# Kernel tuning notes

Hardware: AMD Instinct MI355X
Metric: run time of the kernel (lower is better)

The kernel has to match this reference:

```python
import jax, jax.numpy as jnp
import numpy as np

OBS_LEN, PRED_LEN, N, P = 8, 12, 4096, 32
EH, DH, EMB, BOT, NZ = 64, 128, 64, 1024, 8


def setup_inputs() -> dict:
    key = jax.random.key(0)
    ks = iter(jax.random.split(key, 64))
    rn = lambda shp, s=0.05: (jax.random.normal(next(ks), shp, jnp.float32) * s)
    d = {
        'obs_traj': rn((OBS_LEN, N, 2), 1.0),
        'obs_traj_rel': rn((OBS_LEN, N, 2), 0.5),
        'obs_speed': jax.random.uniform(next(ks), (OBS_LEN, N, 1), jnp.float32),
        'noise': rn((N, NZ), 1.0),
        'enc_emb_W': rn((2, EMB)), 'enc_emb_b': jnp.zeros((EMB,), jnp.float32),
        'enc_Wih': rn((EMB, 4 * EH)), 'enc_Whh': rn((EH, 4 * EH)), 'enc_b': jnp.zeros((4 * EH,), jnp.float32),
        'pool_sp_W': rn((2, 64)), 'pool_sp_b': jnp.zeros((64,), jnp.float32),
        'pool_spd_W': rn((1, 64)), 'pool_spd_b': jnp.zeros((64,), jnp.float32),
        'pool_l1_W': rn((192, 512)), 'pool_l1_b': jnp.zeros((512,), jnp.float32),
        'pool_bn1_g': jnp.ones((512,), jnp.float32), 'pool_bn1_b': jnp.zeros((512,), jnp.float32),
        'pool_l2_W': rn((512, BOT)), 'pool_l2_b': jnp.zeros((BOT,), jnp.float32),
        'pool_bn2_g': jnp.ones((BOT,), jnp.float32), 'pool_bn2_b': jnp.zeros((BOT,), jnp.float32),
        'spd_emb_W': rn((OBS_LEN, 64)), 'spd_emb_b': jnp.zeros((64,), jnp.float32),
        'ctx_l1_W': rn((EH + BOT + 64, 1024)), 'ctx_l1_b': jnp.zeros((1024,), jnp.float32),
        'ctx_bn1_g': jnp.ones((1024,), jnp.float32), 'ctx_bn1_b': jnp.zeros((1024,), jnp.float32),
        'ctx_l2_W': rn((1024, DH - NZ)), 'ctx_l2_b': jnp.zeros((DH - NZ,), jnp.float32),
        'ctx_bn2_g': jnp.ones((DH - NZ,), jnp.float32), 'ctx_bn2_b': jnp.zeros((DH - NZ,), jnp.float32),
        'dec_emb_W': rn((3, EMB)), 'dec_emb_b': jnp.zeros((EMB,), jnp.float32),
        'dec_Wih': rn((EMB, 4 * DH)), 'dec_Whh': rn((DH, 4 * DH)), 'dec_b': jnp.zeros((4 * DH,), jnp.float32),
        'h2p_W': rn((DH, 2)), 'h2p_b': jnp.zeros((2,), jnp.float32),
        'group_size': P,
    }
    return d


def _lstm(xs, Wih, Whh, b, h0, c0):
    # xs: [T, B, in]; PyTorch gate order (i, f, g, o)
    def step(carry, x):
        h, c = carry
        g = x @ Wih + h @ Whh + b
        i, f, gg, o = jnp.split(g, 4, axis=-1)
        c = jax.nn.sigmoid(f) * c + jax.nn.sigmoid(i) * jnp.tanh(gg)
        h = jax.nn.sigmoid(o) * jnp.tanh(c)
        return (h, c), h
    (h, c), _ = jax.lax.scan(step, (h0, c0), xs)
    return h, c


def _bn(x, g, b):
    # BatchNorm1d, eval mode with running_mean=0, running_var=1
    return x * g + b


def reference(obs_traj, obs_traj_rel, obs_speed, noise,
              enc_emb_W, enc_emb_b, enc_Wih, enc_Whh, enc_b,
              pool_sp_W, pool_sp_b, pool_spd_W, pool_spd_b,
              pool_l1_W, pool_l1_b, pool_bn1_g, pool_bn1_b,
              pool_l2_W, pool_l2_b, pool_bn2_g, pool_bn2_b,
              spd_emb_W, spd_emb_b,
              ctx_l1_W, ctx_l1_b, ctx_bn1_g, ctx_bn1_b,
              ctx_l2_W, ctx_l2_b, ctx_bn2_g, ctx_bn2_b,
              dec_emb_W, dec_emb_b, dec_Wih, dec_Whh, dec_b,
              h2p_W, h2p_b, group_size):
    n = obs_traj.shape[1]
    G = n // group_size
    # ---- Encoder: embed rel traj, run LSTM, take final hidden ----
    emb = obs_traj_rel @ enc_emb_W + enc_emb_b                       # [T, N, 64]
    h0 = jnp.zeros((n, EH), emb.dtype)
    final_h, _ = _lstm(emb, enc_Wih, enc_Whh, enc_b, h0, h0)         # [N, 64]
    # ---- PoolHiddenNet (vectorized per-group P x P social pooling) ----
    end_pos = obs_traj[-1].reshape(G, group_size, 2)                 # [G, P, 2]
    end_spd = obs_speed[-1].reshape(G, group_size, 1)                # [G, P, 1]
    hG = final_h.reshape(G, group_size, EH)                          # [G, P, 64]
    # rel[g, i, j] = pos[g, j] - pos[g, i]
    rel = end_pos[:, None, :, :] - end_pos[:, :, None, :]            # [G, P, P, 2]
    rel_e = rel @ pool_sp_W + pool_sp_b                              # [G, P, P, 64]
    spd_e = end_spd @ pool_spd_W + pool_spd_b                        # [G, P, 64]
    Pn = group_size
    feat = jnp.concatenate([
        rel_e,
        jnp.broadcast_to(hG[:, None, :, :], (G, Pn, Pn, EH)),
        jnp.broadcast_to(spd_e[:, None, :, :], (G, Pn, Pn, 64)),
    ], axis=-1)                                                      # [G, P, P, 192]
    h1 = jax.nn.relu(_bn(feat @ pool_l1_W + pool_l1_b, pool_bn1_g, pool_bn1_b))
    h2 = jax.nn.relu(_bn(h1 @ pool_l2_W + pool_l2_b, pool_bn2_g, pool_bn2_b))
    pool_h = jnp.max(h2, axis=2).reshape(n, BOT)                     # max over j -> [N, 1024]
    # ---- speed context: sigmoid(Linear(8 -> 64)) over obs speed history ----
    spd_hist = jnp.transpose(obs_speed[:, :, 0])                     # [N, 8]
    speed_ctx = jax.nn.sigmoid(spd_hist @ spd_emb_W + spd_emb_b)     # [N, 64]
    # ---- mlp_decoder_context + ped-level noise ----
    ctx_in = jnp.concatenate([final_h, pool_h, speed_ctx], axis=1)   # [N, 1152]
    c1 = jax.nn.relu(_bn(ctx_in @ ctx_l1_W + ctx_l1_b, ctx_bn1_g, ctx_bn1_b))
    ctx = jax.nn.relu(_bn(c1 @ ctx_l2_W + ctx_l2_b, ctx_bn2_g, ctx_bn2_b))  # [N, 120]
    dec_h = jnp.concatenate([ctx, noise], axis=1)                    # [N, 128]
    dec_c = jnp.zeros_like(dec_h)
    # ---- Decoder rollout (pred_len steps) ----
    last_pos = obs_traj[-1]
    last_speed = obs_speed[-1]                                       # [N, 1]
    x0 = jnp.concatenate([obs_traj_rel[-1], last_speed], axis=1) @ dec_emb_W + dec_emb_b

    def step(carry, _):
        h, c, x, lp = carry
        g = x @ dec_Wih + h @ dec_Whh + dec_b
        i, f, gg, o = jnp.split(g, 4, axis=-1)
        c = jax.nn.sigmoid(f) * c + jax.nn.sigmoid(i) * jnp.tanh(gg)
        h = jax.nn.sigmoid(o) * jnp.tanh(c)
        rel_pos = h @ h2p_W + h2p_b                                  # [N, 2]
        cur = rel_pos + lp
        x = jnp.concatenate([rel_pos, last_speed], axis=1) @ dec_emb_W + dec_emb_b
        return (h, c, x, cur), rel_pos

    _, rels = jax.lax.scan(step, (dec_h, dec_c, x0, last_pos), None, length=PRED_LEN)
    return rels  # [pred_len, N, 2]
```

## Files before the change

kernel.cpp:

```cpp
#include <hip/hip_runtime.h>

typedef __attribute__((ext_vector_type(8))) short v8s;
typedef __attribute__((ext_vector_type(4))) float v4f;
typedef unsigned short u16;

#define DINL static __device__ __forceinline__

DINL float b2f(u16 u){ union { unsigned uu; float ff; } x; x.uu = ((unsigned)u)<<16; return x.ff; }
DINL u16 f2b(float f){ union { float ff; unsigned uu; } x; x.ff = f; unsigned r = x.uu + 0x7FFFu + ((x.uu>>16)&1u); return (u16)(r>>16); }
DINL float sigm(float x){ return 1.0f/(1.0f+__expf(-x)); }
DINL float tanh_(float x){ return 2.0f/(1.0f+__expf(-2.0f*x)) - 1.0f; }
DINL float ld(const void* p, int i, int isf){
    return isf ? ((const float*)p)[i] : b2f(((const u16*)p)[i]);
}
DINL void g2lds16(const u16* g, u16* l){
    __builtin_amdgcn_global_load_lds(
        (const __attribute__((address_space(1))) unsigned int*)g,
        (__attribute__((address_space(3))) unsigned int*)l, 16, 0, 0);
}

#define FLAG_OFF 0x000000
#define AUX_OFF  0x000100
#define ENCF_OFF 0x010000
#define DECF_OFF 0x020000
#define CW2T_OFF 0x050000
#define W2T_OFF  0x090000
#define DECH_OFF 0x090000
#define CW1T_OFF 0x190000
#define IT_OFF   0x3D0000
#define IR_OFF   0x3F0000
#define IS_OFF   0x410000
#define INZ_OFF  0x420000
#define IW1H_OFF 0x430000
#define SM_OFF   0x440000
#define CTX_OFF  0x450000
#define AV_OFF   0xD50000
#define BIG_NEED 0x1550000

#define SM_EEW 0
#define SM_EEB 128
#define SM_ENB 192
#define SM_DEW 448
#define SM_DEB 640
#define SM_DNB 704
#define SM_H2W 1216
#define SM_H2B 1472
#define SM_SEW 1536
#define SM_SEB 2048

__global__ void k_detect(const void* obs_speed, int* flag){
    if (threadIdx.x == 0 && blockIdx.x == 0){
        const u16* p = (const u16*)obs_speed;
        int f = 0;
        for (int i = 0; i < 16; ++i){
            u16 v = p[2*i];
            if ((v & 0x8000u) || v > 0x3F80u) f = 1;
        }
        *flag = f;
    }
}

__global__ __launch_bounds__(256) void k_conv_inp(
    const void* obs_traj, const void* obs_rel, const void* obs_speed, const void* noise,
    const void* pool_l1_W,
    const void* eeW, const void* eeB, const void* encB,
    const void* deW, const void* deB, const void* decB,
    const void* h2W, const void* h2B, const void* seW, const void* seB,
    const int* flag, u16* IT, u16* IR, u16* IS, u16* INZ, u16* IW1H, u16* SM)
{
    const int isf = *flag;
    int idx = blockIdx.x*256 + threadIdx.x;
    if (idx < 65536){ IT[idx] = f2b(ld(obs_traj, idx, isf)); return; }
    idx -= 65536;
    if (idx < 65536){ IR[idx] = f2b(ld(obs_rel, idx, isf)); return; }
    idx -= 65536;
    if (idx < 32768){ IS[idx] = f2b(ld(obs_speed, idx, isf)); return; }
    idx -= 32768;
    if (idx < 32768){ INZ[idx] = f2b(ld(noise, idx, isf)); return; }
    idx -= 32768;
    if (idx < 32768){ IW1H[idx] = f2b(ld(pool_l1_W, idx + 32768, isf)); return; }
    idx -= 32768;
    if (idx < 128){ SM[SM_EEW + idx] = f2b(ld(eeW, idx, isf)); return; }
    idx -= 128;
    if (idx < 64){ SM[SM_EEB + idx] = f2b(ld(eeB, idx, isf)); return; }
    idx -= 64;
    if (idx < 256){ SM[SM_ENB + idx] = f2b(ld(encB, idx, isf)); return; }
    idx -= 256;
    if (idx < 192){ SM[SM_DEW + idx] = f2b(ld(deW, idx, isf)); return; }
    idx -= 192;
    if (idx < 64){ SM[SM_DEB + idx] = f2b(ld(deB, idx, isf)); return; }
    idx -= 64;
    if (idx < 512){ SM[SM_DNB + idx] = f2b(ld(decB, idx, isf)); return; }
    idx -= 512;
    if (idx < 256){ SM[SM_H2W + idx] = f2b(ld(h2W, idx, isf)); return; }
    idx -= 256;
    if (idx < 2){ SM[SM_H2B + idx] = f2b(ld(h2B, idx, isf)); return; }
    idx -= 2;
    if (idx < 512){ SM[SM_SEW + idx] = f2b(ld(seW, idx, isf)); return; }
    idx -= 512;
    if (idx < 64){ SM[SM_SEB + idx] = f2b(ld(seB, idx, isf)); return; }
}

__global__ __launch_bounds__(256) void k_trans(
    const void* __restrict__ in, u16* __restrict__ out,
    int K, int N, const int* __restrict__ flag)
{
    __shared__ float tile[64][65];
    const int isf = *flag;
    const int nbase = blockIdx.x*64, kbase = blockIdx.y*64;
    const int c = threadIdx.x & 63, r0 = (threadIdx.x >> 6)*16;
    for (int rep = 0; rep < 16; ++rep){
        int r = r0 + rep;
        int n = nbase + c;
        float v = 0.f;
        if (n < N) v = ld(in, (kbase + r)*N + n, isf);
        tile[r][c] = v;
    }
    __syncthreads();
    for (int rep = 0; rep < 16; ++rep){
        int r = r0 + rep;
        out[(size_t)(nbase + r)*K + kbase + c] = f2b(tile[c][r]);
    }
}

__global__ __launch_bounds__(256) void k_prep_frag(
    const void* __restrict__ enc_Wih, const void* __restrict__ enc_Whh,
    const void* __restrict__ dec_Wih, const void* __restrict__ dec_Whh,
    const int* flag, u16* __restrict__ encF, u16* __restrict__ decF)
{
    const int isf = *flag;
    int idx = blockIdx.x*256 + threadIdx.x;
    if (idx < 32768){
        int jj = idx&7, lane = (idx>>3)&63, kcnf = idx>>9;
        int kc = kcnf&3, nf = kcnf>>2;
        int k = kc*32 + (lane>>4)*8 + jj, n = nf*16 + (lane&15);
        encF[idx] = (k < 64) ? f2b(ld(enc_Wih, k*256+n, isf)) : f2b(ld(enc_Whh, (k-64)*256+n, isf));
        return;
    }
    idx -= 32768;
    {
        int jj = idx&7, lane = (idx>>3)&63, kcnf = idx>>9;
        int kc = kcnf % 6, nf = kcnf / 6;
        int k = kc*32 + (lane>>4)*8 + jj, n = nf*16 + (lane&15);
        decF[idx] = (k < 64) ? f2b(ld(dec_Wih, k*512+n, isf)) : f2b(ld(dec_Whh, (k-64)*512+n, isf));
    }
}

__global__ __launch_bounds__(256) void k_prep_small(
    const void* __restrict__ spW, const void* __restrict__ spB,
    const void* __restrict__ spdW, const void* __restrict__ spdB,
    const void* __restrict__ l1W, const void* __restrict__ l1B,
    const void* __restrict__ bn1g, const void* __restrict__ bn1b,
    const void* __restrict__ l2b, const void* __restrict__ bn2g, const void* __restrict__ bn2b,
    const void* __restrict__ c1b, const void* __restrict__ cbn1g, const void* __restrict__ cbn1b,
    const void* __restrict__ c2b, const void* __restrict__ cbn2g, const void* __restrict__ cbn2b,
    const int* flag, float* __restrict__ AUX)
{
    const int isf = *flag;
    int idx = blockIdx.x*256 + threadIdx.x;
    if (idx < 512){
        int c = idx;
        float m0 = 0.f, m1 = 0.f, qv = 0.f, cv = 0.f;
        for (int e = 0; e < 64; ++e){
            float w1a = ld(l1W, e*512 + c, isf);
            m0 += ld(spW, e, isf)*w1a;
            m1 += ld(spW, 64+e, isf)*w1a;
            cv += ld(spB, e, isf)*w1a;
            float w1c = ld(l1W, (128+e)*512 + c, isf);
            qv += ld(spdW, e, isf)*w1c;
            cv += ld(spdB, e, isf)*w1c;
        }
        cv += ld(l1B, c, isf);
        float g1 = ld(bn1g, c, isf), bb1 = ld(bn1b, c, isf);
        AUX[c] = m0; AUX[512+c] = m1; AUX[1024+c] = qv; AUX[1536+c] = cv;
        AUX[2048+c] = g1; AUX[2560+c] = bb1;
        AUX[3072+c] = g1*m0; AUX[3584+c] = g1*m1;
        return;
    }
    idx -= 512;
    if (idx < 1024){
        float g = ld(bn2g, idx, isf);
        AUX[4096+idx] = g; AUX[5120+idx] = ld(l2b, idx, isf)*g + ld(bn2b, idx, isf);
        return;
    }
    idx -= 1024;
    if (idx < 1024){
        float g = ld(cbn1g, idx, isf);
        AUX[6144+idx] = g; AUX[7168+idx] = ld(c1b, idx, isf)*g + ld(cbn1b, idx, isf);
        return;
    }
    idx -= 1024;
    if (idx < 128){
        int c = idx;
        float g  = (c < 120) ? ld(cbn2g, c, isf) : 1.f;
        float bb = (c < 120) ? (ld(c2b, c, isf)*g + ld(cbn2b, c, isf)) : 0.f;
        AUX[8192+c] = g; AUX[8320+c] = bb;
    }
}

__global__ __launch_bounds__(256) void k_encoder(
    const u16* __restrict__ rel, const u16* __restrict__ embW, const u16* __restrict__ embB,
    const u16* __restrict__ encF, const u16* __restrict__ encB,
    u16* __restrict__ ctxIn)
{
    __shared__ __align__(16) u16 Als[16*136];
    const int t = threadIdx.x, pedbase = blockIdx.x*16;
    const int w = t>>6, lane = t&63, quad = lane>>4, l15 = lane&15;
    for (int idx = t; idx < 16*64; idx += 256){ int p = idx>>6, jj = idx&63; Als[p*136 + 64 + jj] = 0; }
    {
        int p = t>>4, e0 = (t&15)*4;
        float rx = b2f(rel[(pedbase+p)*2 + 0]);
        float ry = b2f(rel[(pedbase+p)*2 + 1]);
        for (int e = e0; e < e0+4; ++e)
            Als[p*136 + e] = f2b(rx*b2f(embW[e]) + ry*b2f(embW[64+e]) + b2f(embB[e]));
    }
    const int j = w*16 + l15;
    const float bi = b2f(encB[j]), bff = b2f(encB[64+j]), bg = b2f(encB[128+j]), bo = b2f(encB[192+j]);
    float c4[4] = {0.f,0.f,0.f,0.f};
    for (int step = 0; step < 8; ++step){
        __syncthreads();
        v4f acc[4];
        for (int q = 0; q < 4; ++q) acc[q] = (v4f){0.f,0.f,0.f,0.f};
        for (int kc = 0; kc < 4; ++kc){
            v8s a = *(const v8s*)&Als[l15*136 + kc*32 + quad*8];
            for (int q = 0; q < 4; ++q){
                int nf = q*4 + w;
                v8s b = *(const v8s*)&encF[((nf*4 + kc)*64 + lane)*8];
                acc[q] = __builtin_amdgcn_mfma_f32_16x16x32_bf16(a, b, acc[q], 0, 0, 0);
            }
        }
        __syncthreads();
        for (int r = 0; r < 4; ++r){
            float gi = sigm(acc[0][r] + bi), gf = sigm(acc[1][r] + bff);
            float gg = tanh_(acc[2][r] + bg), go = sigm(acc[3][r] + bo);
            c4[r] = gf*c4[r] + gi*gg;
            Als[(quad*4 + r)*136 + 64 + j] = f2b(go*tanh_(c4[r]));
        }
        if (step < 7){
            int p = t>>4, e0 = (t&15)*4;
            float rx = b2f(rel[(step+1)*8192 + (pedbase+p)*2 + 0]);
            float ry = b2f(rel[(step+1)*8192 + (pedbase+p)*2 + 1]);
            for (int e = e0; e < e0+4; ++e)
                Als[p*136 + e] = f2b(rx*b2f(embW[e]) + ry*b2f(embW[64+e]) + b2f(embB[e]));
        }
    }
    __syncthreads();
    for (int idx = t; idx < 1024; idx += 256){
        int p = idx>>6, e = idx&63;
        ctxIn[(size_t)(pedbase+p)*1152 + e] = Als[p*136 + 64 + e];
    }
}

__global__ __launch_bounds__(256) void k_avec(
    const u16* __restrict__ ctxIn, const u16* __restrict__ obs_traj,
    const u16* __restrict__ obs_speed, const u16* __restrict__ IW1H,
    const u16* __restrict__ sW, const u16* __restrict__ sB,
    const float* __restrict__ AUX, u16* __restrict__ Avec, u16* __restrict__ ctxOut)
{
    __shared__ float hs[8][64];
    __shared__ float pxs[8], pys[8], sps[8];
    const int t = threadIdx.x, pedbase = blockIdx.x*8;
    for (int idx = t; idx < 512; idx += 256){
        int p = idx>>6, e = idx&63;
        hs[p][e] = b2f(ctxIn[(size_t)(pedbase+p)*1152 + e]);
    }
    if (t < 8){
        pxs[t] = b2f(obs_traj[7*8192 + (pedbase+t)*2 + 0]);
        pys[t] = b2f(obs_traj[7*8192 + (pedbase+t)*2 + 1]);
        sps[t] = b2f(obs_speed[7*4096 + pedbase + t]);
    }
    __syncthreads();
    const int c0 = (t&127)*4, pg = (t>>7)*4;
    float4 acc[4];
    for (int p = 0; p < 4; ++p) acc[p] = make_float4(0.f,0.f,0.f,0.f);
    for (int e = 0; e < 64; ++e){
        ushort4 wv = *(const ushort4*)(IW1H + e*512 + c0);
        float w0 = b2f(wv.x), w1 = b2f(wv.y), w2 = b2f(wv.z), w3 = b2f(wv.w);
        for (int p = 0; p < 4; ++p){
            float h = hs[pg+p][e];
            acc[p].x += h*w0; acc[p].y += h*w1; acc[p].z += h*w2; acc[p].w += h*w3;
        }
    }
    float4 m0 = *(const float4*)(AUX + c0),        m1 = *(const float4*)(AUX + 512 + c0);
    float4 qv = *(const float4*)(AUX + 1024 + c0), cv = *(const float4*)(AUX + 1536 + c0);
    float4 g1 = *(const float4*)(AUX + 2048 + c0), bb = *(const float4*)(AUX + 2560 + c0);
    for (int p = 0; p < 4; ++p){
        float px = pxs[pg+p], py = pys[pg+p], sp = sps[pg+p];
        ushort4 o;
        o.x = f2b(g1.x*(px*m0.x + py*m1.x + sp*qv.x + cv.x + acc[p].x) + bb.x);
        o.y = f2b(g1.y*(px*m0.y + py*m1.y + sp*qv.y + cv.y + acc[p].y) + bb.y);
        o.z = f2b(g1.z*(px*m0.z + py*m1.z + sp*qv.z + cv.z + acc[p].z) + bb.z);
        o.w = f2b(g1.w*(px*m0.w + py*m1.w + sp*qv.w + cv.w + acc[p].w) + bb.w);
        *(ushort4*)&Avec[(size_t)(pedbase+pg+p)*512 + c0] = o;
    }
    {
        int s = t & 63;
        for (int rep = 0; rep < 2; ++rep){
            int p = (t>>6)*2 + rep;
            int nid = pedbase + p;
            float a = b2f(sB[s]);
            for (int tt = 0; tt < 8; ++tt) a += b2f(obs_speed[tt*4096 + nid]) * b2f(sW[tt*64 + s]);
            ctxOut[(size_t)nid*1152 + 1088 + s] = f2b(sigm(a));
        }
    }
}

__global__ __launch_bounds__(256, 2) void k_pool(
    const u16* __restrict__ Avec, const u16* __restrict__ W2T,
    const u16* __restrict__ IT, const float* __restrict__ AUX,
    u16* __restrict__ ctxIn)
{
    __shared__ __align__(16) u16 Als[64*72];
    __shared__ __align__(16) u16 Bls[512*64];
    __shared__ float auxM[1024];
    __shared__ float pxs[2], pys[2];
    const int t = threadIdx.x;
    const int g = blockIdx.x >> 4, ip = blockIdx.x & 15;
    const int n0 = blockIdx.y * 512;
    const int w = t>>6, lane = t&63, quad = lane>>4, l15 = lane&15;
    const int rw = w>>1, cw = w&1;
    const int aj = t>>3, ao = t&7;
    for (int i = t; i < 1024; i += 256) auxM[i] = AUX[3072 + i];
    if (t < 2){
        pxs[t] = b2f(IT[7*8192 + (g*32 + ip*2 + t)*2 + 0]);
        pys[t] = b2f(IT[7*8192 + (g*32 + ip*2 + t)*2 + 1]);
    }
    const int lgr = (lane&7) ^ (lane>>3);
    const u16* bsrc = W2T + (size_t)(n0 + w*8 + (lane>>3))*512 + lgr*8;
    u16* bdst = &Bls[w*512];
    const u16* arow = Avec + (size_t)(g*32+aj)*512 + ao*8;
    v4f acc[2][16];
    for (int mf = 0; mf < 2; ++mf) for (int nf = 0; nf < 16; ++nf) acc[mf][nf] = (v4f){0.f,0.f,0.f,0.f};
    for (int ch = 0; ch < 8; ++ch){
        const int k0 = ch*64;
        __syncthreads();
        for (int it = 0; it < 16; ++it)
            g2lds16(bsrc + k0 + it*16384, bdst + it*2048);
        {
            union { v8s v; u16 u[8]; } av;
            av.v = *(const v8s*)(arow + k0);
            float a[8], m0a[8], m1a[8];
            for (int i = 0; i < 8; ++i){
                a[i] = b2f(av.u[i]);
                m0a[i] = auxM[k0 + ao*8 + i];
                m1a[i] = auxM[512 + k0 + ao*8 + i];
            }
            for (int il = 0; il < 2; ++il){
                float npx = -pxs[il], npy = -pys[il];
                union { v8s v; u16 u[8]; } pk;
                for (int i = 0; i < 8; ++i){
                    float v = __builtin_fmaf(npy, m1a[i], __builtin_fmaf(npx, m0a[i], a[i]));
                    pk.u[i] = f2b(fmaxf(v, 0.f));
                }
                *(v8s*)&Als[(il*32+aj)*72 + ao*8] = pk.v;
            }
        }
        __syncthreads();
        for (int kc = 0; kc < 2; ++kc){
            v8s af[2];
            for (int mf = 0; mf < 2; ++mf)
                af[mf] = *(const v8s*)&Als[(rw*32 + mf*16 + l15)*72 + kc*32 + quad*8];
            const int pq = ((kc*4 + quad) ^ (l15&7))*8;
            const u16* bbase = &Bls[(cw*256 + l15)*64 + pq];
            #pragma unroll
            for (int nf = 0; nf < 16; ++nf){
                v8s bf = *(const v8s*)(bbase + nf*1024);
                acc[0][nf] = __builtin_amdgcn_mfma_f32_16x16x32_bf16(af[0], bf, acc[0][nf], 0, 0, 0);
                acc[1][nf] = __builtin_amdgcn_mfma_f32_16x16x32_bf16(af[1], bf, acc[1][nf], 0, 0, 0);
            }
        }
    }
    const float* S2 = AUX + 4096; const float* B2 = AUX + 5120;
    for (int nf = 0; nf < 16; ++nf){
        int n = n0 + cw*256 + nf*16 + l15;
        float s = S2[n], bb = B2[n];
        float mm = 0.f;
        for (int mf = 0; mf < 2; ++mf)
            for (int r = 0; r < 4; ++r)
                mm = fmaxf(mm, fmaxf(s*acc[mf][nf][r] + bb, 0.f));
        mm = fmaxf(mm, __shfl_xor(mm, 16));
        mm = fmaxf(mm, __shfl_xor(mm, 32));
        if (quad == 0) ctxIn[(size_t)(g*32 + ip*2 + rw)*1152 + 64 + n] = f2b(mm);
    }
}

template<int MF>
__global__ __launch_bounds__(256) void k_gemm_bt(
    const u16* __restrict__ A, int lda, const u16* __restrict__ BT,
    const float* __restrict__ S, const float* __restrict__ Bb,
    u16* __restrict__ out, int ldo, int K, int validN,
    const u16* __restrict__ noisep)
{
    __shared__ __align__(16) u16 Als[MF*32*72];
    __shared__ __align__(16) u16 Bls[128*72];
    const int t = threadIdx.x;
    const int m0 = blockIdx.x*(MF*32), n0 = blockIdx.y*128;
    const int w = t>>6, lane = t&63, quad = lane>>4, l15 = lane&15;
    const int rw = w>>1, cw = w&1;
    v4f acc[MF][4];
    for (int mf = 0; mf < MF; ++mf) for (int nf = 0; nf < 4; ++nf) acc[mf][nf] = (v4f){0.f,0.f,0.f,0.f};
    const int nch = K >> 6;
    for (int ch = 0; ch < nch; ++ch){
        const int k0 = ch*64;
        __syncthreads();
        if (MF == 4){
// ... 87 lines not shown
        v4f acc[4][2];
        for (int q = 0; q < 4; ++q) for (int nfl = 0; nfl < 2; ++nfl) acc[q][nfl] = (v4f){0.f,0.f,0.f,0.f};
        for (int kc = 0; kc < 6; ++kc){
            v8s a = *(const v8s*)&Als[l15*200 + kc*32 + quad*8];
            for (int q = 0; q < 4; ++q){
                for (int nfl = 0; nfl < 2; ++nfl){
                    int nf = q*8 + w*2 + nfl;
                    v8s b = *(const v8s*)&decF[((nf*6 + kc)*64 + lane)*8];
                    acc[q][nfl] = __builtin_amdgcn_mfma_f32_16x16x32_bf16(a, b, acc[q][nfl], 0, 0, 0);
                }
            }
        }
        __syncthreads();
        for (int nfl = 0; nfl < 2; ++nfl){
            int j = w*32 + nfl*16 + l15;
            for (int r = 0; r < 4; ++r){
                float gi = sigm(acc[0][nfl][r] + bI[nfl]), gf = sigm(acc[1][nfl][r] + bF[nfl]);
                float gg = tanh_(acc[2][nfl][r] + bG[nfl]), go = sigm(acc[3][nfl][r] + bO[nfl]);
                c8[nfl][r] = gf*c8[nfl][r] + gi*gg;
                Als[(quad*4 + r)*200 + 64 + j] = f2b(go*tanh_(c8[nfl][r]));
            }
        }
        __syncthreads();
        if (t < 32){
            int p = t>>1, cmp = t&1;
            float rp = b2f(h2pB[cmp]);
            for (int jj = 0; jj < 128; ++jj) rp += b2f(Als[p*200 + 64 + jj]) * h2ps[jj*2 + cmp];
            int oi = s*8192 + (pedbase+p)*2 + cmp;
            if (isf) ((float*)outp)[oi] = rp;
            else     ((u16*)outp)[oi]   = f2b(rp);
            rps[p][cmp] = rp;
        }
        __syncthreads();
        {
            int p = t>>4, e0 = (t&15)*4;
            for (int e = e0; e < e0+4; ++e){
                float v = rps[p][0]*b2f(dembW[e]) + rps[p][1]*b2f(dembW[64+e]) + sps[p]*b2f(dembW[128+e]) + b2f(dembB[e]);
                Als[p*200 + e] = f2b(v);
            }
        }
    }
}

extern "C" void kernel_launch(void* const* d_in, const int* in_sizes, int n_in,
                              void* d_out, int out_size, void* d_ws, size_t ws_size,
                              hipStream_t stream)
{
    (void)in_sizes; (void)n_in; (void)out_size;
    const void* obs_traj  = d_in[0];
    const void* obs_rel   = d_in[1];
    const void* obs_speed = d_in[2];
    const void* noise     = d_in[3];
    const void* enc_emb_W = d_in[4];
    const void* enc_emb_b = d_in[5];
// ... 30 lines not shown
    const void* h2p_W     = d_in[36];
    const void* h2p_b     = d_in[37];

    char* ws = (char*)d_ws;
    int*   flag  = (int*)  (ws + FLAG_OFF);
    float* AUX   = (float*)(ws + AUX_OFF);
    u16*   encF  = (u16*)  (ws + ENCF_OFF);
    u16*   decF  = (u16*)  (ws + DECF_OFF);
    u16*   cW2T  = (u16*)  (ws + CW2T_OFF);
    u16*   W2T   = (u16*)  (ws + W2T_OFF);
    u16*   decH  = (u16*)  (ws + DECH_OFF);
    u16*   cW1T  = (u16*)  (ws + CW1T_OFF);
    u16*   IT    = (u16*)  (ws + IT_OFF);
    u16*   IR    = (u16*)  (ws + IR_OFF);
    u16*   IS    = (u16*)  (ws + IS_OFF);
    u16*   INZ   = (u16*)  (ws + INZ_OFF);
    u16*   IW1H  = (u16*)  (ws + IW1H_OFF);
    u16*   SM    = (u16*)  (ws + SM_OFF);
    u16*   ctxIn = (u16*)  (ws + CTX_OFF);
    u16*   Avec  = (u16*)  (ws + AV_OFF);
    u16*   c1    = (u16*)  (ws + AV_OFF);
    const bool big = (ws_size >= (size_t)BIG_NEED);

    k_detect<<<dim3(1), dim3(64), 0, stream>>>(obs_speed, flag);
    k_conv_inp<<<dim3(905), dim3(256), 0, stream>>>(
        obs_traj, obs_rel, obs_speed, noise, pool_l1_W,
        enc_emb_W, enc_emb_b, enc_b, dec_emb_W, dec_emb_b, dec_b,
        h2p_W, h2p_b, spd_emb_W, spd_emb_b,
        flag, IT, IR, IS, INZ, IW1H, SM);
    k_prep_frag<<<dim3(512), dim3(256), 0, stream>>>(
        enc_Wih, enc_Whh, dec_Wih, dec_Whh, flag, encF, decF);
    k_trans<<<dim3(16, 8),  dim3(256), 0, stream>>>(pool_l2_W, W2T, 512, 1024, flag);
    k_trans<<<dim3(16, 18), dim3(256), 0, stream>>>(ctx_l1_W, cW1T, 1152, 1024, flag);
    k_trans<<<dim3(2, 16),  dim3(256), 0, stream>>>(ctx_l2_W, cW2T, 1024, 120, flag);
    k_prep_small<<<dim3(11), dim3(256), 0, stream>>>(
        pool_sp_W, pool_sp_b, pool_spd_W, pool_spd_b,
        pool_l1_W, pool_l1_b, pool_bn1_g, pool_bn1_b,
        pool_l2_b, pool_bn2_g, pool_bn2_b,
        ctx_l1_b, ctx_bn1_g, ctx_bn1_b,
        ctx_l2_b, ctx_bn2_g, ctx_bn2_b, flag, AUX);
    k_encoder<<<dim3(256), dim3(256), 0, stream>>>(
        IR, SM + SM_EEW, SM + SM_EEB, encF, SM + SM_ENB, ctxIn);
    k_avec<<<dim3(512), dim3(256), 0, stream>>>(
        ctxIn, IT, IS, IW1H, SM + SM_SEW, SM + SM_SEB, AUX, Avec, ctxIn);
    k_pool<<<dim3(2048, 2), dim3(256), 0, stream>>>(Avec, W2T, IT, AUX, ctxIn);
    if (big){
        k_gemm_bt<4><<<dim3(32, 8), dim3(256), 0, stream>>>(
            ctxIn, 1152, cW1T, AUX + 6144, AUX + 7168, c1, 1024, 1152, 1024, (const u16*)nullptr);
        k_gemm_bt<2><<<dim3(64, 1), dim3(256), 0, stream>>>(
            c1, 1024, cW2T, AUX + 8192, AUX + 8320, decH, 128, 1024, 120, INZ);
    } else {
        k_gemm_bt<4><<<dim3(16, 8), dim3(256), 0, stream>>>(
            ctxIn, 1152, cW1T, AUX + 6144, AUX + 7168, c1, 1024, 1152, 1024, (const u16*)nullptr);
        k_gemm_bt<2><<<dim3(32, 1), dim3(256), 0, stream>>>(
            c1, 1024, cW2T, AUX + 8192, AUX + 8320, decH, 128, 1024, 120, INZ);
        k_gemm_bt<4><<<dim3(16, 8), dim3(256), 0, stream>>>(
            ctxIn + (size_t)2048*1152, 1152, cW1T, AUX + 6144, AUX + 7168, c1, 1024, 1152, 1024, (const u16*)nullptr);
        k_gemm_bt<2><<<dim3(32, 1), dim3(256), 0, stream>>>(
            c1, 1024, cW2T, AUX + 8192, AUX + 8320, decH + (size_t)2048*128, 128, 1024, 120, INZ + (size_t)2048*8);
    }
    k_decoder<<<dim3(256), dim3(256), 0, stream>>>(
        decH, decF, SM + SM_DNB, SM + SM_DEW, SM + SM_DEB,
        SM + SM_H2W, SM + SM_H2B, IR, IS, flag, d_out);
}
```

Before: 507.7 us.

## Merge prep kernels into one launch, fuse avec into encoder, retile pool

Replaces the detect, convert, fragment-prep, three transpose and small-prep launches with a single k_prep kernel where each block detects the dtype flag itself. Folds the avec computation into the encoder so the hidden state stays in LDS instead of a round trip through global memory. Retiles k_pool to 256 output columns per block with a 4x4 MFMA tile per wave, prefetches the next A chunk, and uses a cheaper round-half-up bf16 conversion. Also parallelises the decoder's h2p dot product across 256 threads with shuffle reductions. The aim is fewer launches and better occupancy; the pool retile doubles the grid and repeats the A-side prologue work per block.

```diff
diff --git a/kernel.cpp b/kernel.cpp
--- a/kernel.cpp
+++ b/kernel.cpp
@@ -8,6 +8,7 @@
 
 DINL float b2f(u16 u){ union { unsigned uu; float ff; } x; x.uu = ((unsigned)u)<<16; return x.ff; }
 DINL u16 f2b(float f){ union { float ff; unsigned uu; } x; x.ff = f; unsigned r = x.uu + 0x7FFFu + ((x.uu>>16)&1u); return (u16)(r>>16); }
+DINL u16 f2b_hu(float f){ union { float ff; unsigned uu; } x; x.ff = f; return (u16)((x.uu + 0x8000u)>>16); }
 DINL float sigm(float x){ return 1.0f/(1.0f+__expf(-x)); }
 DINL float tanh_(float x){ return 2.0f/(1.0f+__expf(-2.0f*x)) - 1.0f; }
 DINL float ld(const void* p, int i, int isf){
@@ -17,6 +18,15 @@
     __builtin_amdgcn_global_load_lds(
         (const __attribute__((address_space(1))) unsigned int*)g,
         (__attribute__((address_space(3))) unsigned int*)l, 16, 0, 0);
+}
+DINL int detect_isf(const void* obs_speed){
+    const u16* p = (const u16*)obs_speed;
+    int f = 0;
+    for (int i = 0; i < 16; ++i){
+        u16 v = p[2*i];
+        if ((v & 0x8000u) || v > 0x3F80u) f = 1;
+    }
+    return f;
 }
 
 #define FLAG_OFF 0x000000
@@ -48,67 +58,11 @@
 #define SM_SEW 1536
 #define SM_SEB 2048
 
-__global__ void k_detect(const void* obs_speed, int* flag){
-    if (threadIdx.x == 0 && blockIdx.x == 0){
-        const u16* p = (const u16*)obs_speed;
-        int f = 0;
-        for (int i = 0; i < 16; ++i){
-            u16 v = p[2*i];
-            if ((v & 0x8000u) || v > 0x3F80u) f = 1;
-        }
-        *flag = f;
-    }
-}
-
-__global__ __launch_bounds__(256) void k_conv_inp(
-    const void* obs_traj, const void* obs_rel, const void* obs_speed, const void* noise,
-    const void* pool_l1_W,
-    const void* eeW, const void* eeB, const void* encB,
-    const void* deW, const void* deB, const void* decB,
-    const void* h2W, const void* h2B, const void* seW, const void* seB,
-    const int* flag, u16* IT, u16* IR, u16* IS, u16* INZ, u16* IW1H, u16* SM)
+DINL void trans_tile(const void* in, u16* out, int K, int N, int isf,
+                     int bx, int by, int t, float tile[64][65])
 {
-    const int isf = *flag;
-    int idx = blockIdx.x*256 + threadIdx.x;
-    if (idx < 65536){ IT[idx] = f2b(ld(obs_traj, idx, isf)); return; }
-    idx -= 65536;
-    if (idx < 65536){ IR[idx] = f2b(ld(obs_rel, idx, isf)); return; }
-    idx -= 65536;
-    if (idx < 32768){ IS[idx] = f2b(ld(obs_speed, idx, isf)); return; }
-    idx -= 32768;
-    if (idx < 32768){ INZ[idx] = f2b(ld(noise, idx, isf)); return; }
-    idx -= 32768;
-    if (idx < 32768){ IW1H[idx] = f2b(ld(pool_l1_W, idx + 32768, isf)); return; }
-    idx -= 32768;
-    if (idx < 128){ SM[SM_EEW + idx] = f2b(ld(eeW, idx, isf)); return; }
-    idx -= 128;
-    if (idx < 64){ SM[SM_EEB + idx] = f2b(ld(eeB, idx, isf)); return; }
-    idx -= 64;
-    if (idx < 256){ SM[SM_ENB + idx] = f2b(ld(encB, idx, isf)); return; }
-    idx -= 256;
-    if (idx < 192){ SM[SM_DEW + idx] = f2b(ld(deW, idx, isf)); return; }
-    idx -= 192;
-    if (idx < 64){ SM[SM_DEB + idx] = f2b(ld(deB, idx, isf)); return; }
-    idx -= 64;
-    if (idx < 512){ SM[SM_DNB + idx] = f2b(ld(decB, idx, isf)); return; }
-    idx -= 512;
-    if (idx < 256){ SM[SM_H2W + idx] = f2b(ld(h2W, idx, isf)); return; }
-    idx -= 256;
-    if (idx < 2){ SM[SM_H2B + idx] = f2b(ld(h2B, idx, isf)); return; }
-    idx -= 2;
-    if (idx < 512){ SM[SM_SEW + idx] = f2b(ld(seW, idx, isf)); return; }
-    idx -= 512;
-    if (idx < 64){ SM[SM_SEB + idx] = f2b(ld(seB, idx, isf)); return; }
-}
-
-__global__ __launch_bounds__(256) void k_trans(
-    const void* __restrict__ in, u16* __restrict__ out,
-    int K, int N, const int* __restrict__ flag)
-{
-    __shared__ float tile[64][65];
-    const int isf = *flag;
-    const int nbase = blockIdx.x*64, kbase = blockIdx.y*64;
-    const int c = threadIdx.x & 63, r0 = (threadIdx.x >> 6)*16;
+    const int nbase = bx*64, kbase = by*64;
+    const int c = t & 63, r0 = (t >> 6)*16;
     for (int rep = 0; rep < 16; ++rep){
         int r = r0 + rep;
         int n = nbase + c;
@@ -123,90 +77,150 @@
     }
 }
 
-__global__ __launch_bounds__(256) void k_prep_frag(
-    const void* __restrict__ enc_Wih, const void* __restrict__ enc_Whh,
-    const void* __restrict__ dec_Wih, const void* __restrict__ dec_Whh,
-    const int* flag, u16* __restrict__ encF, u16* __restrict__ decF)
+__global__ __launch_bounds__(256) void k_prep(
+    const void* obs_traj, const void* obs_rel, const void* obs_speed, const void* noise,
+    const void* eeW, const void* eeB, const void* enc_Wih, const void* enc_Whh, const void* encB,
+    const void* spW, const void* spB, const void* spdW, const void* spdB,
+    const void* pool_l1_W, const void* l1B, const void* bn1g, const void* bn1b,
+    const void* pool_l2_W, const void* l2b, const void* bn2g, const void* bn2b,
+    const void* seW, const void* seB,
+    const void* ctx_l1_W, const void* c1b, const void* cbn1g, const void* cbn1b,
+    const void* ctx_l2_W, const void* c2b, const void* cbn2g, const void* cbn2b,
+    const void* deW, const void* deB, const void* dec_Wih, const void* dec_Whh, const void* decB,
+    const void* h2W, const void* h2B,
+    int* flag, float* AUX,
+    u16* IT, u16* IR, u16* IS, u16* INZ, u16* IW1H, u16* SM,
+    u16* W2T, u16* cW1T, u16* cW2T, u16* encF, u16* decF)
 {
-    const int isf = *flag;
-    int idx = blockIdx.x*256 + threadIdx.x;
-    if (idx < 32768){
-        int jj = idx&7, lane = (idx>>3)&63, kcnf = idx>>9;
-        int kc = kcnf&3, nf = kcnf>>2;
-        int k = kc*32 + (lane>>4)*8 + jj, n = nf*16 + (lane&15);
-        encF[idx] = (k < 64) ? f2b(ld(enc_Wih, k*256+n, isf)) : f2b(ld(enc_Whh, (k-64)*256+n, isf));
+    __shared__ float tile[64][65];
+    __shared__ int sisf;
+    const int t = threadIdx.x;
+    if (t == 0){
+        int f = detect_isf(obs_speed);
+        sisf = f;
+        if (blockIdx.x == 0) *flag = f;
+    }
+    __syncthreads();
+    const int isf = sisf;
+    int bid = blockIdx.x;
+    if (bid < 905){
+        int idx = bid*256 + t;
+        if (idx < 65536){ IT[idx] = f2b(ld(obs_traj, idx, isf)); return; }
+        idx -= 65536;
+        if (idx < 65536){ IR[idx] = f2b(ld(obs_rel, idx, isf)); return; }
+        idx -= 65536;
+        if (idx < 32768){ IS[idx] = f2b(ld(obs_speed, idx, isf)); return; }
+        idx -= 32768;
+        if (idx < 32768){ INZ[idx] = f2b(ld(noise, idx, isf)); return; }
+        idx -= 32768;
+        if (idx < 32768){ IW1H[idx] = f2b(ld(pool_l1_W, idx + 32768, isf)); return; }
+        idx -= 32768;
+        if (idx < 128){ SM[SM_EEW + idx] = f2b(ld(eeW, idx, isf)); return; }
+        idx -= 128;
+        if (idx < 64){ SM[SM_EEB + idx] = f2b(ld(eeB, idx, isf)); return; }
+        idx -= 64;
+        if (idx < 256){ SM[SM_ENB + idx] = f2b(ld(encB, idx, isf)); return; }
+        idx -= 256;
+        if (idx < 192){ SM[SM_DEW + idx] = f2b(ld(deW, idx, isf)); return; }
+        idx -= 192;
+        if (idx < 64){ SM[SM_DEB + idx] = f2b(ld(deB, idx, isf)); return; }
+        idx -= 64;
+        if (idx < 512){ SM[SM_DNB + idx] = f2b(ld(decB, idx, isf)); return; }
+        idx -= 512;
+        if (idx < 256){ SM[SM_H2W + idx] = f2b(ld(h2W, idx, isf)); return; }
+        idx -= 256;
+        if (idx < 2){ SM[SM_H2B + idx] = f2b(ld(h2B, idx, isf)); return; }
+        idx -= 2;
+        if (idx < 512){ SM[SM_SEW + idx] = f2b(ld(seW, idx, isf)); return; }
+        idx -= 512;
+        if (idx < 64){ SM[SM_SEB + idx] = f2b(ld(seB, idx, isf)); return; }
         return;
     }
-    idx -= 32768;
+    bid -= 905;
+    if (bid < 512){
+        int idx = bid*256 + t;
+        if (idx < 32768){
+            int jj = idx&7, lane = (idx>>3)&63, kcnf = idx>>9;
+            int kc = kcnf&3, nf = kcnf>>2;
+            int k = kc*32 + (lane>>4)*8 + jj, n = nf*16 + (lane&15);
+            encF[idx] = (k < 64) ? f2b(ld(enc_Wih, k*256+n, isf)) : f2b(ld(enc_Whh, (k-64)*256+n, isf));
+        } else {
+            idx -= 32768;
+            int jj = idx&7, lane = (idx>>3)&63, kcnf = idx>>9;
+            int kc = kcnf % 6, nf = kcnf / 6;
+            int k = kc*32 + (lane>>4)*8 + jj, n = nf*16 + (lane&15);
+            decF[idx] = (k < 64) ? f2b(ld(dec_Wih, k*512+n, isf)) : f2b(ld(dec_Whh, (k-64)*512+n, isf));
+        }
+        return;
+    }
+    bid -= 512;
+    if (bid < 128){ trans_tile(pool_l2_W, W2T, 512, 1024, isf, bid & 15, bid >> 4, t, tile); return; }
+    bid -= 128;
+    if (bid < 288){ trans_tile(ctx_l1_W, cW1T, 1152, 1024, isf, bid & 15, bid >> 4, t, tile); return; }
+    bid -= 288;
+    if (bid < 32){ trans_tile(ctx_l2_W, cW2T, 1024, 120, isf, bid & 1, bid >> 1, t, tile); return; }
+    bid -= 32;
     {
-        int jj = idx&7, lane = (idx>>3)&63, kcnf = idx>>9;
-        int kc = kcnf % 6, nf = kcnf / 6;
-        int k = kc*32 + (lane>>4)*8 + jj, n = nf*16 + (lane&15);
-        decF[idx] = (k < 64) ? f2b(ld(dec_Wih, k*512+n, isf)) : f2b(ld(dec_Whh, (k-64)*512+n, isf));
-    }
-}
-
-__global__ __launch_bounds__(256) void k_prep_small(
-    const void* __restrict__ spW, const void* __restrict__ spB,
-    const void* __restrict__ spdW, const void* __restrict__ spdB,
-    const void* __restrict__ l1W, const void* __restrict__ l1B,
-    const void* __restrict__ bn1g, const void* __restrict__ bn1b,
-    const void* __restrict__ l2b, const void* __restrict__ bn2g, const void* __restrict__ bn2b,
-    const void* __restrict__ c1b, const void* __restrict__ cbn1g, const void* __restrict__ cbn1b,
-    const void* __restrict__ c2b, const void* __restrict__ cbn2g, const void* __restrict__ cbn2b,
-    const int* flag, float* __restrict__ AUX)
-{
-    const int isf = *flag;
-    int idx = blockIdx.x*256 + threadIdx.x;
-    if (idx < 512){
-        int c = idx;
-        float m0 = 0.f, m1 = 0.f, qv = 0.f, cv = 0.f;
-        for (int e = 0; e < 64; ++e){
-            float w1a = ld(l1W, e*512 + c, isf);
-            m0 += ld(spW, e, isf)*w1a;
-            m1 += ld(spW, 64+e, isf)*w1a;
-            cv += ld(spB, e, isf)*w1a;
-            float w1c = ld(l1W, (128+e)*512 + c, isf);
-            qv += ld(spdW, e, isf)*w1c;
-            cv += ld(spdB, e, isf)*w1c;
-        }
-        cv += ld(l1B, c, isf);
-        float g1 = ld(bn1g, c, isf), bb1 = ld(bn1b, c, isf);
-        AUX[c] = m0; AUX[512+c] = m1; AUX[1024+c] = qv; AUX[1536+c] = cv;
-        AUX[2048+c] = g1; AUX[2560+c] = bb1;
-        AUX[3072+c] = g1*m0; AUX[3584+c] = g1*m1;
-        return;
-    }
-    idx -= 512;
-    if (idx < 1024){
-        float g = ld(bn2g, idx, isf);
-        AUX[4096+idx] = g; AUX[5120+idx] = ld(l2b, idx, isf)*g + ld(bn2b, idx, isf);
-        return;
-    }
-    idx -= 1024;
-    if (idx < 1024){
-        float g = ld(cbn1g, idx, isf);
-        AUX[6144+idx] = g; AUX[7168+idx] = ld(c1b, idx, isf)*g + ld(cbn1b, idx, isf);
-        return;
-    }
-    idx -= 1024;
-    if (idx < 128){
-        int c = idx;
-        float g  = (c < 120) ? ld(cbn2g, c, isf) : 1.f;
-        float bb = (c < 120) ? (ld(c2b, c, isf)*g + ld(cbn2b, c, isf)) : 0.f;
-        AUX[8192+c] = g; AUX[8320+c] = bb;
+        int idx = bid*256 + t;
+        if (idx < 512){
+            int c = idx;
+            float m0 = 0.f, m1 = 0.f, qv = 0.f, cv = 0.f;
+            for (int e = 0; e < 64; ++e){
+                float w1a = ld(pool_l1_W, e*512 + c, isf);
+                m0 += ld(spW, e, isf)*w1a;
+                m1 += ld(spW, 64+e, isf)*w1a;
+                cv += ld(spB, e, isf)*w1a;
+                float w1c = ld(pool_l1_W, (128+e)*512 + c, isf);
+                qv += ld(spdW, e, isf)*w1c;
+                cv += ld(spdB, e, isf)*w1c;
+            }
+            cv += ld(l1B, c, isf);
+            float g1 = ld(bn1g, c, isf), bb1 = ld(bn1b, c, isf);
+            AUX[c] = m0; AUX[512+c] = m1; AUX[1024+c] = qv; AUX[1536+c] = cv;
+            AUX[2048+c] = g1; AUX[2560+c] = bb1;
+            AUX[3072+c] = g1*m0; AUX[3584+c] = g1*m1;
+            return;
+        }
+        idx -= 512;
+        if (idx < 1024){
+            float g = ld(bn2g, idx, isf);
+            AUX[4096+idx] = g; AUX[5120+idx] = ld(l2b, idx, isf)*g + ld(bn2b, idx, isf);
+            return;
+        }
+        idx -= 1024;
+        if (idx < 1024){
+            float g = ld(cbn1g, idx, isf);
+            AUX[6144+idx] = g; AUX[7168+idx] = ld(c1b, idx, isf)*g + ld(cbn1b, idx, isf);
+            return;
+        }
+        idx -= 1024;
+        if (idx < 128){
+            int c = idx;
+            float g  = (c < 120) ? ld(cbn2g, c, isf) : 1.f;
+            float bb = (c < 120) ? (ld(c2b, c, isf)*g + ld(cbn2b, c, isf)) : 0.f;
+            AUX[8192+c] = g; AUX[8320+c] = bb;
+        }
     }
 }
 
 __global__ __launch_bounds__(256) void k_encoder(
     const u16* __restrict__ rel, const u16* __restrict__ embW, const u16* __restrict__ embB,
     const u16* __restrict__ encF, const u16* __restrict__ encB,
-    u16* __restrict__ ctxIn)
+    const u16* __restrict__ IT, const u16* __restrict__ IS, const u16* __restrict__ IW1H,
+    const u16* __restrict__ sW, const u16* __restrict__ sB,
+    const float* __restrict__ AUX,
+    u16* __restrict__ ctxIn, u16* __restrict__ Avec)
 {
     __shared__ __align__(16) u16 Als[16*136];
+    __shared__ float pxs[16], pys[16], sps[16];
     const int t = threadIdx.x, pedbase = blockIdx.x*16;
     const int w = t>>6, lane = t&63, quad = lane>>4, l15 = lane&15;
     for (int idx = t; idx < 16*64; idx += 256){ int p = idx>>6, jj = idx&63; Als[p*136 + 64 + jj] = 0; }
+    if (t < 16){
+        pxs[t] = b2f(IT[7*8192 + (pedbase+t)*2 + 0]);
+        pys[t] = b2f(IT[7*8192 + (pedbase+t)*2 + 1]);
+        sps[t] = b2f(IS[7*4096 + pedbase + t]);
+    }
     {
         int p = t>>4, e0 = (t&15)*4;
         float rx = b2f(rel[(pedbase+p)*2 + 0]);
@@ -249,138 +263,119 @@
         int p = idx>>6, e = idx&63;
         ctxIn[(size_t)(pedbase+p)*1152 + e] = Als[p*136 + 64 + e];
     }
-}
-
-__global__ __launch_bounds__(256) void k_avec(
-    const u16* __restrict__ ctxIn, const u16* __restrict__ obs_traj,
-    const u16* __restrict__ obs_speed, const u16* __restrict__ IW1H,
-    const u16* __restrict__ sW, const u16* __restrict__ sB,
-    const float* __restrict__ AUX, u16* __restrict__ Avec, u16* __restrict__ ctxOut)
-{
-    __shared__ float hs[8][64];
-    __shared__ float pxs[8], pys[8], sps[8];
-    const int t = threadIdx.x, pedbase = blockIdx.x*8;
-    for (int idx = t; idx < 512; idx += 256){
-        int p = idx>>6, e = idx&63;
-        hs[p][e] = b2f(ctxIn[(size_t)(pedbase+p)*1152 + e]);
-    }
-    if (t < 8){
-        pxs[t] = b2f(obs_traj[7*8192 + (pedbase+t)*2 + 0]);
-        pys[t] = b2f(obs_traj[7*8192 + (pedbase+t)*2 + 1]);
-        sps[t] = b2f(obs_speed[7*4096 + pedbase + t]);
-    }
-    __syncthreads();
-    const int c0 = (t&127)*4, pg = (t>>7)*4;
-    float4 acc[4];
-    for (int p = 0; p < 4; ++p) acc[p] = make_float4(0.f,0.f,0.f,0.f);
-    for (int e = 0; e < 64; ++e){
-        ushort4 wv = *(const ushort4*)(IW1H + e*512 + c0);
-        float w0 = b2f(wv.x), w1 = b2f(wv.y), w2 = b2f(wv.z), w3 = b2f(wv.w);
-        for (int p = 0; p < 4; ++p){
-            float h = hs[pg+p][e];
-            acc[p].x += h*w0; acc[p].y += h*w1; acc[p].z += h*w2; acc[p].w += h*w3;
-        }
-    }
-    float4 m0 = *(const float4*)(AUX + c0),        m1 = *(const float4*)(AUX + 512 + c0);
-    float4 qv = *(const float4*)(AUX + 1024 + c0), cv = *(const float4*)(AUX + 1536 + c0);
-    float4 g1 = *(const float4*)(AUX + 2048 + c0), bb = *(const float4*)(AUX + 2560 + c0);
-    for (int p = 0; p < 4; ++p){
-        float px = pxs[pg+p], py = pys[pg+p], sp = sps[pg+p];
-        ushort4 o;
-        o.x = f2b(g1.x*(px*m0.x + py*m1.x + sp*qv.x + cv.x + acc[p].x) + bb.x);
-        o.y = f2b(g1.y*(px*m0.y + py*m1.y + sp*qv.y + cv.y + acc[p].y) + bb.y);
-        o.z = f2b(g1.z*(px*m0.z + py*m1.z + sp*qv.z + cv.z + acc[p].z) + bb.z);
-        o.w = f2b(g1.w*(px*m0.w + py*m1.w + sp*qv.w + cv.w + acc[p].w) + bb.w);
-        *(ushort4*)&Avec[(size_t)(pedbase+pg+p)*512 + c0] = o;
+    {
+        const int c0 = (t&127)*4, pg = (t>>7)*8;
+        float4 acc[8];
+        for (int p = 0; p < 8; ++p) acc[p] = make_float4(0.f,0.f,0.f,0.f);
+        for (int e = 0; e < 64; ++e){
+            ushort4 wv = *(const ushort4*)(IW1H + e*512 + c0);
+            float w0 = b2f(wv.x), w1 = b2f(wv.y), w2 = b2f(wv.z), w3 = b2f(wv.w);
+            for (int p = 0; p < 8; ++p){
+                float h = b2f(Als[(pg+p)*136 + 64 + e]);
+                acc[p].x += h*w0; acc[p].y += h*w1; acc[p].z += h*w2; acc[p].w += h*w3;
+            }
+        }
+        float4 m0 = *(const float4*)(AUX + c0),        m1 = *(const float4*)(AUX + 512 + c0);
+        float4 qv = *(const float4*)(AUX + 1024 + c0), cv = *(const float4*)(AUX + 1536 + c0);
+        float4 g1 = *(const float4*)(AUX + 2048 + c0), bb = *(const float4*)(AUX + 2560 + c0);
+        for (int p = 0; p < 8; ++p){
+            float px = pxs[pg+p], py = pys[pg+p], sp = sps[pg+p];
+            ushort4 o;
+            o.x = f2b(g1.x*(px*m0.x + py*m1.x + sp*qv.x + cv.x + acc[p].x) + bb.x);
+            o.y = f2b(g1.y*(px*m0.y + py*m1.y + sp*qv.y + cv.y + acc[p].y) + bb.y);
+            o.z = f2b(g1.z*(px*m0.z + py*m1.z + sp*qv.z + cv.z + acc[p].z) + bb.z);
+            o.w = f2b(g1.w*(px*m0.w + py*m1.w + sp*qv.w + cv.w + acc[p].w) + bb.w);
+            *(ushort4*)&Avec[(size_t)(pedbase+pg+p)*512 + c0] = o;
+        }
     }
     {
         int s = t & 63;
-        for (int rep = 0; rep < 2; ++rep){
-            int p = (t>>6)*2 + rep;
+        for (int rep = 0; rep < 4; ++rep){
+            int p = (t>>6)*4 + rep;
             int nid = pedbase + p;
             float a = b2f(sB[s]);
-            for (int tt = 0; tt < 8; ++tt) a += b2f(obs_speed[tt*4096 + nid]) * b2f(sW[tt*64 + s]);
-            ctxOut[(size_t)nid*1152 + 1088 + s] = f2b(sigm(a));
-        }
-    }
-}
-
-__global__ __launch_bounds__(256, 2) void k_pool(
+            for (int tt = 0; tt < 8; ++tt) a += b2f(IS[tt*4096 + nid]) * b2f(sW[tt*64 + s]);
+            ctxIn[(size_t)nid*1152 + 1088 + s] = f2b(sigm(a));
+        }
+    }
+}
+
+__global__ __launch_bounds__(256, 3) void k_pool(
     const u16* __restrict__ Avec, const u16* __restrict__ W2T,
     const u16* __restrict__ IT, const float* __restrict__ AUX,
     u16* __restrict__ ctxIn)
 {
     __shared__ __align__(16) u16 Als[64*72];
-    __shared__ __align__(16) u16 Bls[512*64];
+    __shared__ __align__(16) u16 Bls[256*64];
     __shared__ float auxM[1024];
     __shared__ float pxs[2], pys[2];
     const int t = threadIdx.x;
     const int g = blockIdx.x >> 4, ip = blockIdx.x & 15;
-    const int n0 = blockIdx.y * 512;
+    const int n0 = blockIdx.y * 256;
     const int w = t>>6, lane = t&63, quad = lane>>4, l15 = lane&15;
-    const int rw = w>>1, cw = w&1;
     const int aj = t>>3, ao = t&7;
     for (int i = t; i < 1024; i += 256) auxM[i] = AUX[3072 + i];
     if (t < 2){
         pxs[t] = b2f(IT[7*8192 + (g*32 + ip*2 + t)*2 + 0]);
         pys[t] = b2f(IT[7*8192 + (g*32 + ip*2 + t)*2 + 1]);
     }
-    const int lgr = (lane&7) ^ (lane>>3);
-    const u16* bsrc = W2T + (size_t)(n0 + w*8 + (lane>>3))*512 + lgr*8;
+    const u16* bsrc = W2T + (size_t)(n0 + w*8 + (lane>>3))*512 + (size_t)(((lane&7) ^ (lane>>3)))*8;
     u16* bdst = &Bls[w*512];
     const u16* arow = Avec + (size_t)(g*32+aj)*512 + ao*8;
-    v4f acc[2][16];
-    for (int mf = 0; mf < 2; ++mf) for (int nf = 0; nf < 16; ++nf) acc[mf][nf] = (v4f){0.f,0.f,0.f,0.f};
+    v4f acc[4][4];
+    for (int mf = 0; mf < 4; ++mf) for (int nf = 0; nf < 4; ++nf) acc[mf][nf] = (v4f){0.f,0.f,0.f,0.f};
+    union { v8s v; u16 u[8]; } av;
+    av.v = *(const v8s*)arow;
     for (int ch = 0; ch < 8; ++ch){
         const int k0 = ch*64;
         __syncthreads();
-        for (int it = 0; it < 16; ++it)
+        for (int it = 0; it < 8; ++it)
             g2lds16(bsrc + k0 + it*16384, bdst + it*2048);
         {
-            union { v8s v; u16 u[8]; } av;
-            av.v = *(const v8s*)(arow + k0);
-            float a[8], m0a[8], m1a[8];
-            for (int i = 0; i < 8; ++i){
-                a[i] = b2f(av.u[i]);
-                m0a[i] = auxM[k0 + ao*8 + i];
-                m1a[i] = auxM[512 + k0 + ao*8 + i];
-            }
+            float a0[8], m0a[8], m1a[8];
+            for (int i = 0; i < 8; ++i) a0[i] = b2f(av.u[i]);
+            *(float4*)(m0a)   = *(const float4*)&auxM[k0 + ao*8];
+            *(float4*)(m0a+4) = *(const float4*)&auxM[k0 + ao*8 + 4];
+            *(float4*)(m1a)   = *(const float4*)&auxM[512 + k0 + ao*8];
+            *(float4*)(m1a+4) = *(const float4*)&auxM[512 + k0 + ao*8 + 4];
             for (int il = 0; il < 2; ++il){
                 float npx = -pxs[il], npy = -pys[il];
                 union { v8s v; u16 u[8]; } pk;
                 for (int i = 0; i < 8; ++i){
-                    float v = __builtin_fmaf(npy, m1a[i], __builtin_fmaf(npx, m0a[i], a[i]));
-                    pk.u[i] = f2b(fmaxf(v, 0.f));
+                    float v = __builtin_fmaf(npy, m1a[i], __builtin_fmaf(npx, m0a[i], a0[i]));
+                    pk.u[i] = f2b_hu(fmaxf(v, 0.f));
                 }
                 *(v8s*)&Als[(il*32+aj)*72 + ao*8] = pk.v;
             }
         }
+        if (ch < 7) av.v = *(const v8s*)(arow + (ch+1)*64);
         __syncthreads();
         for (int kc = 0; kc < 2; ++kc){
-            v8s af[2];
-            for (int mf = 0; mf < 2; ++mf)
-                af[mf] = *(const v8s*)&Als[(rw*32 + mf*16 + l15)*72 + kc*32 + quad*8];
-            const int pq = ((kc*4 + quad) ^ (l15&7))*8;
-            const u16* bbase = &Bls[(cw*256 + l15)*64 + pq];
+            v8s af[4];
+            for (int mf = 0; mf < 4; ++mf)
+                af[mf] = *(const v8s*)&Als[(mf*16 + l15)*72 + kc*32 + quad*8];
+            const int sl = ((kc*4 + quad) ^ (l15&7))*8;
             #pragma unroll
-            for (int nf = 0; nf < 16; ++nf){
-                v8s bf = *(const v8s*)(bbase + nf*1024);
+            for (int nf = 0; nf < 4; ++nf){
+                v8s bf = *(const v8s*)&Bls[(w*64 + nf*16 + l15)*64 + sl];
                 acc[0][nf] = __builtin_amdgcn_mfma_f32_16x16x32_bf16(af[0], bf, acc[0][nf], 0, 0, 0);
                 acc[1][nf] = __builtin_amdgcn_mfma_f32_16x16x32_bf16(af[1], bf, acc[1][nf], 0, 0, 0);
+                acc[2][nf] = __builtin_amdgcn_mfma_f32_16x16x32_bf16(af[2], bf, acc[2][nf], 0, 0, 0);
+                acc[3][nf] = __builtin_amdgcn_mfma_f32_16x16x32_bf16(af[3], bf, acc[3][nf], 0, 0, 0);
             }
         }
     }
     const float* S2 = AUX + 4096; const float* B2 = AUX + 5120;
-    for (int nf = 0; nf < 16; ++nf){
-        int n = n0 + cw*256 + nf*16 + l15;
+    for (int nf = 0; nf < 4; ++nf){
+        int n = n0 + w*64 + nf*16 + l15;
         float s = S2[n], bb = B2[n];
-        float mm = 0.f;
-        for (int mf = 0; mf < 2; ++mf)
-            for (int r = 0; r < 4; ++r)
-                mm = fmaxf(mm, fmaxf(s*acc[mf][nf][r] + bb, 0.f));
-        mm = fmaxf(mm, __shfl_xor(mm, 16));
-        mm = fmaxf(mm, __shfl_xor(mm, 32));
-        if (quad == 0) ctxIn[(size_t)(g*32 + ip*2 + rw)*1152 + 64 + n] = f2b(mm);
+        float mm0 = 0.f, mm1 = 0.f;
+        for (int mf = 0; mf < 2; ++mf) for (int r = 0; r < 4; ++r) mm0 = fmaxf(mm0, fmaxf(s*acc[mf][nf][r] + bb, 0.f));
+        for (int mf = 2; mf < 4; ++mf) for (int r = 0; r < 4; ++r) mm1 = fmaxf(mm1, fmaxf(s*acc[mf][nf][r] + bb, 0.f));
+        mm0 = fmaxf(mm0, __shfl_xor(mm0, 16)); mm0 = fmaxf(mm0, __shfl_xor(mm0, 32));
+        mm1 = fmaxf(mm1, __shfl_xor(mm1, 16)); mm1 = fmaxf(mm1, __shfl_xor(mm1, 32));
+        if (quad == 0) ctxIn[(size_t)(g*32 + ip*2 + 0)*1152 + 64 + n] = f2b(mm0);
+        if (quad == 1) ctxIn[(size_t)(g*32 + ip*2 + 1)*1152 + 64 + n] = f2b(mm1);
     }
 }
 
@@ -514,14 +509,22 @@
             }
         }
         __syncthreads();
-        if (t < 32){
-            int p = t>>1, cmp = t&1;
-            float rp = b2f(h2pB[cmp]);
-            for (int jj = 0; jj < 128; ++jj) rp += b2f(Als[p*200 + 64 + jj]) * h2ps[jj*2 + cmp];
-            int oi = s*8192 + (pedbase+p)*2 + cmp;
-            if (isf) ((float*)outp)[oi] = rp;
-            else     ((u16*)outp)[oi]   = f2b(rp);
-            rps[p][cmp] = rp;
+        {
+            int p = t>>4, cmp = (t>>3)&1, part = t&7;
+            float rp = 0.f;
+            int j0 = part*16;
+            for (int jj = j0; jj < j0+16; ++jj)
+                rp += b2f(Als[p*200 + 64 + jj]) * h2ps[jj*2 + cmp];
+            rp += __shfl_xor(rp, 1);
+            rp += __shfl_xor(rp, 2);
+            rp += __shfl_xor(rp, 4);
+            if (part == 0){
+                rp += b2f(h2pB[cmp]);
+                int oi = s*8192 + (pedbase+p)*2 + cmp;
+                if (isf) ((float*)outp)[oi] = rp;
+                else     ((u16*)outp)[oi]   = f2b(rp);
+                rps[p][cmp] = rp;
+            }
         }
         __syncthreads();
         {
@@ -598,28 +601,23 @@
     u16*   c1    = (u16*)  (ws + AV_OFF);
     const bool big = (ws_size >= (size_t)BIG_NEED);
 
-    k_detect<<<dim3(1), dim3(64), 0, stream>>>(obs_speed, flag);
-    k_conv_inp<<<dim3(905), dim3(256), 0, stream>>>(
-        obs_traj, obs_rel, obs_speed, noise, pool_l1_W,
-        enc_emb_W, enc_emb_b, enc_b, dec_emb_W, dec_emb_b, dec_b,
-        h2p_W, h2p_b, spd_emb_W, spd_emb_b,
-        flag, IT, IR, IS, INZ, IW1H, SM);
-    k_prep_frag<<<dim3(512), dim3(256), 0, stream>>>(
-        enc_Wih, enc_Whh, dec_Wih, dec_Whh, flag, encF, decF);
-    k_trans<<<dim3(16, 8),  dim3(256), 0, stream>>>(pool_l2_W, W2T, 512, 1024, flag);
-    k_trans<<<dim3(16, 18), dim3(256), 0, stream>>>(ctx_l1_W, cW1T, 1152, 1024, flag);
-    k_trans<<<dim3(2, 16),  dim3(256), 0, stream>>>(ctx_l2_W, cW2T, 1024, 120, flag);
-    k_prep_small<<<dim3(11), dim3(256), 0, stream>>>(
+    k_prep<<<dim3(1876), dim3(256), 0, stream>>>(
+        obs_traj, obs_rel, obs_speed, noise,
+        enc_emb_W, enc_emb_b, enc_Wih, enc_Whh, enc_b,
         pool_sp_W, pool_sp_b, pool_spd_W, pool_spd_b,
         pool_l1_W, pool_l1_b, pool_bn1_g, pool_bn1_b,
-        pool_l2_b, pool_bn2_g, pool_bn2_b,
-        ctx_l1_b, ctx_bn1_g, ctx_bn1_b,
-        ctx_l2_b, ctx_bn2_g, ctx_bn2_b, flag, AUX);
+        pool_l2_W, pool_l2_b, pool_bn2_g, pool_bn2_b,
+        spd_emb_W, spd_emb_b,
+        ctx_l1_W, ctx_l1_b, ctx_bn1_g, ctx_bn1_b,
+        ctx_l2_W, ctx_l2_b, ctx_bn2_g, ctx_bn2_b,
+        dec_emb_W, dec_emb_b, dec_Wih, dec_Whh, dec_b,
+        h2p_W, h2p_b,
+        flag, AUX, IT, IR, IS, INZ, IW1H, SM,
+        W2T, cW1T, cW2T, encF, decF);
     k_encoder<<<dim3(256), dim3(256), 0, stream>>>(
-        IR, SM + SM_EEW, SM + SM_EEB, encF, SM + SM_ENB, ctxIn);
-    k_avec<<<dim3(512), dim3(256), 0, stream>>>(
-        ctxIn, IT, IS, IW1H, SM + SM_SEW, SM + SM_SEB, AUX, Avec, ctxIn);
-    k_pool<<<dim3(2048, 2), dim3(256), 0, stream>>>(Avec, W2T, IT, AUX, ctxIn);
+        IR, SM + SM_EEW, SM + SM_EEB, encF, SM + SM_ENB,
+        IT, IS, IW1H, SM + SM_SEW, SM + SM_SEB, AUX, ctxIn, Avec);
+    k_pool<<<dim3(2048, 4), dim3(256), 0, stream>>>(Avec, W2T, IT, AUX, ctxIn);
     if (big){
         k_gemm_bt<4><<<dim3(32, 8), dim3(256), 0, stream>>>(
             ctxIn, 1152, cW1T, AUX + 6144, AUX + 7168, c1, 1024, 1152, 1024, (const u16*)nullptr);
```

Result: faster. 439.2 us (median of 2 runs) (-13.5%).
